# Kernel optimization log

Measured on AMD Instinct MI355X. Metric: run time of the kernel, lower is better.

The kernel has to match this reference:

```python
import jax, jax.numpy as jnp
import numpy as np

N_AGENTS = 16
NE = 128
ED = 96          # entity_shape (entity_last_action=False)
HE = 128         # hypernet_embed
MD = 32          # mixing_embed_dim
NH = 4           # attn heads
HD = HE // NH
BS, T = 32, 50


def setup_inputs() -> dict:
    key = jax.random.key(0)
    ks = jax.random.split(key, 20)
    def lin(k, i, o):
        return (jax.random.normal(k, (i, o), jnp.float32) / np.sqrt(i)).astype(jnp.float32)
    inp = {
        "agent_qs": jax.random.normal(ks[0], (BS, T, N_AGENTS), jnp.float32),
        "entities": jax.random.normal(ks[1], (BS, T, NE, ED), jnp.float32),
        "entity_mask": jax.random.uniform(ks[2], (BS, T, NE)) < 0.15,  # True = masked/inactive
    }
    for i, p in enumerate(["w1", "v"]):
        b = 3 + i * 6
        inp[p + "_fc1_w"] = lin(ks[b], ED, HE)
        inp[p + "_fc1_b"] = jnp.zeros((HE,), jnp.float32)
        inp[p + "_attn_in_w"] = lin(ks[b + 1], HE, 3 * HE)   # in_trans (no bias)
        inp[p + "_attn_out_w"] = lin(ks[b + 2], HE, HE)
        inp[p + "_attn_out_b"] = jnp.zeros((HE,), jnp.float32)
        inp[p + "_fc2_w"] = lin(ks[b + 3], HE, MD)
        inp[p + "_fc2_b"] = jnp.zeros((MD,), jnp.float32)
    return inp


def _hypernet(x, emask, fc1_w, fc1_b, in_w, out_w, out_b, fc2_w, fc2_b, mode):
    # x: [B, ne, ed], emask: [B, ne] bool (True = masked)
    B = x.shape[0]
    x1 = jax.nn.relu(x @ fc1_w + fc1_b)                         # [B, ne, HE]
    agent_mask = emask[:, :N_AGENTS]                            # [B, na]
    af = agent_mask.astype(x.dtype)
    ef = emask.astype(x.dtype)
    # attn_mask = 1 - (1-agent)(1-entity); 1 => masked pair
    pre = (1.0 - (1.0 - af)[:, :, None] * (1.0 - ef)[:, None, :]) > 0.5  # [B, na, ne]
    qkv = x1 @ in_w                                             # [B, ne, 3*HE]
    q, k, v = jnp.split(qkv, 3, axis=-1)
    q = q[:, :N_AGENTS].reshape(B, N_AGENTS, NH, HD)
    k = k.reshape(B, NE, NH, HD)
    v = v.reshape(B, NE, NH, HD)
    logits = jnp.einsum('bqhd,bkhd->bhqk', q, k) / np.float32(np.sqrt(HD))
    logits = jnp.where(pre[:, None], jnp.float32(-1e9), logits)
    w = jax.nn.softmax(logits, axis=-1)                         # [B, NH, na, ne]
    # rows where every entity is masked: torch softmax gives NaN -> filled with 0
    all_masked = jnp.all(pre, axis=-1)                          # [B, na]
    w = jnp.where(all_masked[:, None, :, None], 0.0, w)
    attn = jnp.einsum('bhqk,bkhd->bqhd', w, v).reshape(B, N_AGENTS, HE)
    out = attn @ out_w + out_b
    out = jnp.where(agent_mask[:, :, None], 0.0, out)           # post_mask fill
    x3 = out @ fc2_w + fc2_b
    x3 = jnp.where(agent_mask[:, :, None], 0.0, x3)             # [B, na, MD]
    if mode == 'alt_vector':
        return x3.mean(axis=2)                                  # [B, na]
    return x3.mean(axis=(1, 2))                                 # [B]  (scalar mode)


def reference(agent_qs, entities, entity_mask,
              w1_fc1_w, w1_fc1_b, w1_attn_in_w, w1_attn_out_w, w1_attn_out_b, w1_fc2_w, w1_fc2_b,
              v_fc1_w, v_fc1_b, v_attn_in_w, v_attn_out_w, v_attn_out_b, v_fc2_w, v_fc2_b):
    bs, max_t, ne, ed = entities.shape
    ents = entities.reshape(bs * max_t, ne, ed)
    emask = entity_mask.reshape(bs * max_t, ne)
    qs = agent_qs.reshape(-1, N_AGENTS)
    w1 = _hypernet(ents, emask, w1_fc1_w, w1_fc1_b, w1_attn_in_w, w1_attn_out_w,
                   w1_attn_out_b, w1_fc2_w, w1_fc2_b, 'alt_vector')   # [B, na]
    w1 = jnp.abs(w1)                                            # softmax_mixing_weights=False
    v = _hypernet(ents, emask, v_fc1_w, v_fc1_b, v_attn_in_w, v_attn_out_w,
                  v_attn_out_b, v_fc2_w, v_fc2_b, 'scalar')     # [B]
    q_tot = (qs * w1).sum(axis=1) + v
    return q_tot.reshape(bs, max_t, 1)
```

## Files before the change

kernel.cpp:

```cpp
#include <hip/hip_runtime.h>


#define NA 16
#define NEn 128
#define EDm 96
#define ST 136

typedef __attribute__((ext_vector_type(8))) short bf16x8;
typedef __attribute__((ext_vector_type(4))) float f32x4;

#define MFMA(a, b, c) __builtin_amdgcn_mfma_f32_16x16x32_bf16((a), (b), (c), 0, 0, 0)

#define OFF_W1 0
#define OFF_WQ 12288
#define OFF_WK 28672
#define OFF_WV 45056
#define OFF_WO 61440
#define OFF_W2 77824
#define HYPE 81920
#define WS_FLAG_OFF 327680

__device__ __forceinline__ unsigned short f2bf(float f) {
  unsigned u = __float_as_uint(f);
  u += 0x7fffu + ((u >> 16) & 1u);
  return (unsigned short)(u >> 16);
}

__device__ __forceinline__ void ctile_store(unsigned short* dst, int row0,
                                            int col, f32x4 v) {
  unsigned short m0 = f2bf(v[0]), m1 = f2bf(v[1]), m2 = f2bf(v[2]),
                 m3 = f2bf(v[3]);
  unsigned x = (unsigned)m0 | ((unsigned)m1 << 16);
  unsigned y = (unsigned)m2 | ((unsigned)m3 << 16);
  unsigned ox = (unsigned)__shfl_xor((int)x, 1);
  unsigned oy = (unsigned)__shfl_xor((int)y, 1);
  unsigned w0, w1;
  int ra;
  if ((threadIdx.x & 1) == 0) {
    ra = 0;
    w0 = (x & 0xffffu) | (ox << 16);
    w1 = (x >> 16) | (ox & 0xffff0000u);
  } else {
    ra = 2;
    w0 = (oy & 0xffffu) | (y << 16);
    w1 = (oy >> 16) | (y & 0xffff0000u);
  }
  *(unsigned*)(dst + (row0 + ra) * ST + (col & ~1)) = w0;
  *(unsigned*)(dst + (row0 + ra + 1) * ST + (col & ~1)) = w1;
}

__global__ void prep_kernel(const float* __restrict__ w_fc1w,
                            const float* __restrict__ w_inw,
                            const float* __restrict__ w_outw,
                            const float* __restrict__ w_fc2w,
                            const float* __restrict__ v_fc1w,
                            const float* __restrict__ v_inw,
                            const float* __restrict__ v_outw,
                            const float* __restrict__ v_fc2w,
                            const unsigned char* __restrict__ mask,
                            unsigned short* __restrict__ ws,
                            int* __restrict__ flag) {
  if (blockIdx.x == 160) {
    const uint4 v = *(const uint4*)(mask + threadIdx.x * 16);
    const unsigned nz = (v.x | v.y | v.z | v.w) & 0xffffff00u;
    const int any = __syncthreads_or((int)(nz != 0));
    if (threadIdx.x == 0) *flag = (any == 0) ? 1 : 0;
    return;
  }
  const int g = blockIdx.x * 256 + threadIdx.x;
  const int p = (g >= 20480) ? 1 : 0;
  const int off = (g - p * 20480) * 4;
  const float* fc1w = p ? v_fc1w : w_fc1w;
  const float* inw = p ? v_inw : w_inw;
  const float* outw = p ? v_outw : w_outw;
  const float* fc2w = p ? v_fc2w : w_fc2w;
  unsigned short* wsp = ws + p * HYPE;

  float4 v4;
  if (off < OFF_WQ) {
    v4 = *(const float4*)(fc1w + off);
#pragma unroll
    for (int r = 0; r < 4; ++r) {
      const int oe = off + r;
      const int k = oe >> 7, n = oe & 127;
      const int kt = k >> 5, kr = k & 31, j = kr & 7, khi = kr >> 3;
      const int nt = n >> 4, lo = n & 15;
      wsp[OFF_W1 + (nt * 3 + kt) * 512 + (khi * 16 + lo) * 8 + j] =
          f2bf(((const float*)&v4)[r]);
    }
  } else if (off < OFF_WK) {
    const int i = off - OFF_WQ;
    v4 = *(const float4*)(inw + (i >> 7) * 384 + (i & 127));
#pragma unroll
    for (int r = 0; r < 4; ++r) {
      const int ie = i + r;
      const int k = ie >> 7, n = ie & 127;
      const int kt = k >> 5, kr = k & 31, j = kr & 7, khi = kr >> 3;
      const int nt = n >> 4, lo = n & 15;
      wsp[OFF_WQ + (nt * 4 + kt) * 512 + (khi * 16 + lo) * 8 + j] =
          f2bf(((const float*)&v4)[r] * 0.17677669529663687f);
    }
  } else if (off < OFF_WV) {
    const int i = off - OFF_WK;
    v4 = *(const float4*)(inw + (i >> 7) * 384 + 128 + (i & 127));
#pragma unroll
    for (int r = 0; r < 4; ++r) {
      const int ie = i + r;
      const int m = ie >> 7, c = ie & 127;
      const int h = c >> 5, d = c & 31;
      const int nt = m >> 4;
      const int l = (d >> 3) * 16 + (m & 15);
      wsp[OFF_WK + (h * 8 + nt) * 512 + l * 8 + (d & 7)] =
          f2bf(((const float*)&v4)[r]);
    }
  } else if (off < OFF_WO) {
    const int i = off - OFF_WV;
    v4 = *(const float4*)(inw + (i >> 7) * 384 + 256 + (i & 127));
#pragma unroll
    for (int r = 0; r < 4; ++r) {
      const int ie = i + r;
      const int m = ie >> 7, c = ie & 127;
      const int h = c >> 5, d = c & 31;
      const int kt = m >> 5, mr = m & 31, j = mr & 7, mhi = mr >> 3;
      const int mt = d >> 4, lo = d & 15;
      wsp[OFF_WV + ((h * 2 + mt) * 4 + kt) * 512 + (mhi * 16 + lo) * 8 + j] =
          f2bf(((const float*)&v4)[r]);
    }
  } else if (off < OFF_W2) {
    const int i = off - OFF_WO;
    v4 = *(const float4*)(outw + i);
#pragma unroll
    for (int r = 0; r < 4; ++r) {
      const int ie = i + r;
      const int k = ie >> 7, n = ie & 127;
      const int kt = k >> 5, kr = k & 31, j = kr & 7, khi = kr >> 3;
      const int nt = n >> 4, lo = n & 15;
      wsp[OFF_WO + (nt * 4 + kt) * 512 + (khi * 16 + lo) * 8 + j] =
          f2bf(((const float*)&v4)[r]);
    }
  } else {
    const int i = off - OFF_W2;
    v4 = *(const float4*)(fc2w + i);
#pragma unroll
    for (int r = 0; r < 4; ++r) {
      const int ie = i + r;
      const int k = ie >> 5, n = ie & 31;
      const int kt = k >> 5, kr = k & 31, j = kr & 7, khi = kr >> 3;
      const int nt = n >> 4, lo = n & 15;
      wsp[OFF_W2 + (nt * 4 + kt) * 512 + (khi * 16 + lo) * 8 + j] =
          f2bf(((const float*)&v4)[r]);
    }
  }
}

#define SMEM_BYTES 61696

__global__ __launch_bounds__(256, 2) void qmix_mfma(
    const float* __restrict__ agent_qs, const float* __restrict__ entities,
    const unsigned char* __restrict__ emask_g,
    const unsigned short* __restrict__ wsw, const int* __restrict__ mflag,
    const float* __restrict__ w_fc1b, const float* __restrict__ w_outb,
    const float* __restrict__ w_fc2b, const float* __restrict__ v_fc1b,
    const float* __restrict__ v_outb, const float* __restrict__ v_fc2b,
    float* __restrict__ out_g) {
  const int t = threadIdx.x;
  const int wv = t >> 6;
  const int ln = t & 63;
  const int lr = ln & 15;
  const int lq = ln >> 4;
  const int b = blockIdx.x;
  const float* ents = entities + (size_t)b * (NEn * EDm);

  __shared__ __align__(16) unsigned char smem[SMEM_BYTES];
  unsigned short* sx1 = (unsigned short*)smem;
  unsigned short* sQ = sx1 + 17408;
  unsigned short* sqw = sx1 + 19584;
  unsigned short* sW = sx1 + 21760;
  unsigned short* sVT = sx1 + 23936;
  unsigned short* sattn = sx1 + 28288;
  float2* sred = (float2*)(smem + 60928);
  float* sredf = (float*)(smem + 60928);
  float* sres = (float*)(smem + 61440);
  unsigned char* sm = smem + 61568;

  const int is_i32 = *mflag;
  int mv = 1;
  if (t < NEn) {
    if (is_i32)
      mv = (((const int*)emask_g)[(size_t)b * NEn + t] != 0) ? 1 : 0;
    else
      mv = (emask_g[(size_t)b * NEn + t] != 0) ? 1 : 0;
    sm[t] = (unsigned char)mv;
  }
  const int allE = __syncthreads_and(mv);

  for (int p = 0; p < 2; ++p) {
    const unsigned short* wsb = wsw + (size_t)p * HYPE;
    const float* fc1b = p ? v_fc1b : w_fc1b;
    const float* outb = p ? v_outb : w_outb;
    const float* fc2b = p ? v_fc2b : w_fc2b;

    {
#pragma unroll
      for (int mi = 0; mi < 2; ++mi) {
        const int mt = wv * 2 + mi;
        bf16x8 af[3];
        const float* erow = ents + (mt * 16 + lr) * EDm + lq * 8;
#pragma unroll
        for (int kt = 0; kt < 3; ++kt) {
          float4 u = *(const float4*)(erow + kt * 32);
          float4 v = *(const float4*)(erow + kt * 32 + 4);
          bf16x8 a;
          a[0] = (short)f2bf(u.x); a[1] = (short)f2bf(u.y);
          a[2] = (short)f2bf(u.z); a[3] = (short)f2bf(u.w);
          a[4] = (short)f2bf(v.x); a[5] = (short)f2bf(v.y);
          a[6] = (short)f2bf(v.z); a[7] = (short)f2bf(v.w);
          af[kt] = a;
        }
        for (int nt = 0; nt < 8; ++nt) {
          f32x4 acc = {0.f, 0.f, 0.f, 0.f};
          const unsigned short* bp = wsb + OFF_W1 + (nt * 3) * 512 + ln * 8;
#pragma unroll
          for (int kt = 0; kt < 3; ++kt)
            acc = MFMA(af[kt], *(const bf16x8*)(bp + kt * 512), acc);
          const float bias = fc1b[nt * 16 + lr];
          f32x4 r;
          r[0] = fmaxf(acc[0] + bias, 0.f); r[1] = fmaxf(acc[1] + bias, 0.f);
          r[2] = fmaxf(acc[2] + bias, 0.f); r[3] = fmaxf(acc[3] + bias, 0.f);
          ctile_store(sx1, mt * 16 + lq * 4, nt * 16 + lr, r);
        }
      }
    }
    __syncthreads();

    {
      bf16x8 aq[4];
#pragma unroll
      for (int kt = 0; kt < 4; ++kt)
        aq[kt] = *(const bf16x8*)(sx1 + lr * ST + kt * 32 + lq * 8);
#pragma unroll
      for (int ni = 0; ni < 2; ++ni) {
        const int nt = wv * 2 + ni;
        f32x4 acc = {0.f, 0.f, 0.f, 0.f};
        const unsigned short* bp = wsb + OFF_WQ + (nt * 4) * 512 + ln * 8;
#pragma unroll
        for (int kt = 0; kt < 4; ++kt)
          acc = MFMA(aq[kt], *(const bf16x8*)(bp + kt * 512), acc);
        ctile_store(sQ, lq * 4, nt * 16 + lr, acc);
      }
    }
    __syncthreads();

    for (int h = 0; h < 4; ++h) {
      {
        bf16x8 aQ = *(const bf16x8*)(sQ + lr * ST + h * 32 + lq * 8);
#pragma unroll
        for (int ni = 0; ni < 2; ++ni) {
          const int nt = wv * 2 + ni;
          bf16x8 bk =
              *(const bf16x8*)(wsb + OFF_WK + (h * 8 + nt) * 512 + ln * 8);
          f32x4 acc = {0.f, 0.f, 0.f, 0.f};
          acc = MFMA(aQ, bk, acc);
          ctile_store(sqw, lq * 4, nt * 16 + lr, acc);
        }
        bf16x8 av[2][4];
#pragma unroll
        for (int mt = 0; mt < 2; ++mt)
#pragma unroll
          for (int kt = 0; kt < 4; ++kt)
            av[mt][kt] = *(const bf16x8*)(wsb + OFF_WV +
                                          (((h * 2 + mt) * 4) + kt) * 512 +
                                          ln * 8);
#pragma unroll
        for (int ni = 0; ni < 2; ++ni) {
          const int nt = wv * 2 + ni;
          bf16x8 bx[4];
#pragma unroll
          for (int kt = 0; kt < 4; ++kt)
            bx[kt] =
                *(const bf16x8*)(sx1 + (nt * 16 + lr) * ST + kt * 32 + lq * 8);
#pragma unroll
          for (int mt = 0; mt < 2; ++mt) {
            f32x4 acc = {0.f, 0.f, 0.f, 0.f};
#pragma unroll
            for (int kt = 0; kt < 4; ++kt) acc = MFMA(av[mt][kt], bx[kt], acc);
            ctile_store(sVT, mt * 16 + lq * 4, nt * 16 + lr, acc);
          }
        }
      }
      __syncthreads();

      float mx[4], ex0[4], ex1[4];
      {
        bf16x8 aw[4];
#pragma unroll
        for (int kt = 0; kt < 4; ++kt)
          aw[kt] = *(const bf16x8*)(sqw + lr * ST + kt * 32 + lq * 8);
        f32x4 a0 = {0.f, 0.f, 0.f, 0.f}, a1 = {0.f, 0.f, 0.f, 0.f};
        const int nt0 = wv * 2, nt1 = nt0 + 1;
#pragma unroll
        for (int kt = 0; kt < 4; ++kt) {
          bf16x8 b0 =
              *(const bf16x8*)(sx1 + (nt0 * 16 + lr) * ST + kt * 32 + lq * 8);
          bf16x8 b1 =
              *(const bf16x8*)(sx1 + (nt1 * 16 + lr) * ST + kt * 32 + lq * 8);
          a0 = MFMA(aw[kt], b0, a0);
          a1 = MFMA(aw[kt], b1, a1);
        }
        const int e0m = sm[nt0 * 16 + lr], e1m = sm[nt1 * 16 + lr];
        float l0[4], l1[4];
#pragma unroll
        for (int r = 0; r < 4; ++r) {
          l0[r] = e0m ? -1e9f : a0[r];
          l1[r] = e1m ? -1e9f : a1[r];
          mx[r] = fmaxf(l0[r], l1[r]);
        }
#pragma unroll
        for (int k = 1; k < 16; k <<= 1)
#pragma unroll
          for (int r = 0; r < 4; ++r)
            mx[r] = fmaxf(mx[r], __shfl_xor(mx[r], k));
        float sl[4];
#pragma unroll
        for (int r = 0; r < 4; ++r) {
          ex0[r] = __expf(l0[r] - mx[r]);
          ex1[r] = __expf(l1[r] - mx[r]);
          sl[r] = ex0[r] + ex1[r];
        }
#pragma unroll
        for (int k = 1; k < 16; k <<= 1)
#pragma unroll
          for (int r = 0; r < 4; ++r) sl[r] += __shfl_xor(sl[r], k);
        if (lr == 0) {
#pragma unroll
          for (int r = 0; r < 4; ++r)
            sred[wv * 16 + lq * 4 + r] = make_float2(mx[r], sl[r]);
        }
      }
      __syncthreads();

      {
        f32x4 w0v, w1v;
#pragma unroll
        for (int r = 0; r < 4; ++r) {
          const int row = lq * 4 + r;
          float2 p0 = sred[row], p1 = sred[16 + row], p2 = sred[32 + row],
                 p3 = sred[48 + row];
          float M = fmaxf(fmaxf(p0.x, p1.x), fmaxf(p2.x, p3.x));
          float S = __expf(p0.x - M) * p0.y + __expf(p1.x - M) * p1.y +
                    __expf(p2.x - M) * p2.y + __expf(p3.x - M) * p3.y;
          const float sc = ((int)sm[row] | allE) ? 0.f : (1.f / S);
          const float f = __expf(mx[r] - M) * sc;
          w0v[r] = ex0[r] * f;
          w1v[r] = ex1[r] * f;
        }
        ctile_store(sW, lq * 4, wv * 32 + lr, w0v);
        ctile_store(sW, lq * 4, wv * 32 + 16 + lr, w1v);
      }
      __syncthreads();

      if (wv < 2) {
        bf16x8 afr[4];
#pragma unroll
        for (int kt = 0; kt < 4; ++kt)
          afr[kt] = *(const bf16x8*)(sW + lr * ST + kt * 32 + lq * 8);
        f32x4 acc = {0.f, 0.f, 0.f, 0.f};
#pragma unroll
        for (int kt = 0; kt < 4; ++kt) {
          bf16x8 bfr =
              *(const bf16x8*)(sVT + (wv * 16 + lr) * ST + kt * 32 + lq * 8);
          acc = MFMA(afr[kt], bfr, acc);
        }
        ctile_store(sattn, lq * 4, h * 32 + wv * 16 + lr, acc);
      }
      __syncthreads();
    }

    {
      bf16x8 aa[4];
#pragma unroll
      for (int kt = 0; kt < 4; ++kt)
        aa[kt] = *(const bf16x8*)(sattn + lr * ST + kt * 32 + lq * 8);
#pragma unroll
      for (int ni = 0; ni < 2; ++ni) {
        const int nt = wv * 2 + ni;
        f32x4 acc = {0.f, 0.f, 0.f, 0.f};
        const unsigned short* bp = wsb + OFF_WO + (nt * 4) * 512 + ln * 8;
#pragma unroll
        for (int kt = 0; kt < 4; ++kt)
          acc = MFMA(aa[kt], *(const bf16x8*)(bp + kt * 512), acc);
        const float bj = outb[nt * 16 + lr];
        f32x4 r;
        r[0] = acc[0] + bj; r[1] = acc[1] + bj;
        r[2] = acc[2] + bj; r[3] = acc[3] + bj;
        ctile_store(sQ, lq * 4, nt * 16 + lr, r);
      }
    }
    __syncthreads();

    if (wv < 2) {
      bf16x8 ao[4];
#pragma unroll
      for (int kt = 0; kt < 4; ++kt)
        ao[kt] = *(const bf16x8*)(sQ + lr * ST + kt * 32 + lq * 8);
      f32x4 acc = {0.f, 0.f, 0.f, 0.f};
      const unsigned short* bp = wsb + OFF_W2 + (wv * 4) * 512 + ln * 8;
#pragma unroll
      for (int kt = 0; kt < 4; ++kt)
        acc = MFMA(ao[kt], *(const bf16x8*)(bp + kt * 512), acc);
      const float bc = fc2b[wv * 16 + lr];
      float rs[4];
#pragma unroll
      for (int r = 0; r < 4; ++r) {
        const int row = lq * 4 + r;
        rs[r] = sm[row] ? 0.f : (acc[r] + bc);
      }
#pragma unroll
      for (int k = 1; k < 16; k <<= 1)
#pragma unroll
        for (int r = 0; r < 4; ++r) rs[r] += __shfl_xor(rs[r], k);
      if (lr == 0) {
#pragma unroll
        for (int r = 0; r < 4; ++r) sredf[wv * 16 + lq * 4 + r] = rs[r];
      }
    }
    __syncthreads();
    if (t < 16) {
      const float s = sredf[t] + sredf[16 + t];
      if (p == 0)
        sres[t] = fabsf(s) * (1.f / 32.f);
      else
        sres[16 + t] = s;
    }
    __syncthreads();
  }

  if (t == 0) {
    const float* qs = agent_qs + (size_t)b * NA;
    float tot = 0.f, vs = 0.f;
#pragma unroll
    for (int q = 0; q < NA; ++q) {
      tot += qs[q] * sres[q];
      vs += sres[16 + q];
    }
    out_g[b] = tot + vs * (1.f / 512.f);
  }
}

extern "C" void kernel_launch(void* const* d_in, const int* in_sizes, int n_in,
                              void* d_out, int out_size, void* d_ws,
                              size_t ws_size, hipStream_t stream) {
  (void)n_in; (void)out_size; (void)ws_size;
  const int nb = in_sizes[0] / NA;
  unsigned short* wsw = (unsigned short*)d_ws;
  int* mflag = (int*)((char*)d_ws + WS_FLAG_OFF);

  hipLaunchKernelGGL(prep_kernel, dim3(161), dim3(256), 0, stream,
                     (const float*)d_in[3], (const float*)d_in[5],
                     (const float*)d_in[6], (const float*)d_in[8],
                     (const float*)d_in[10], (const float*)d_in[12],
                     (const float*)d_in[13], (const float*)d_in[15],
                     (const unsigned char*)d_in[2], wsw, mflag);
  hipLaunchKernelGGL(qmix_mfma, dim3(nb), dim3(256), 0, stream,
                     (const float*)d_in[0], (const float*)d_in[1],
                     (const unsigned char*)d_in[2], (const unsigned short*)wsw,
                     (const int*)mflag, (const float*)d_in[4],
                     (const float*)d_in[7], (const float*)d_in[9],
                     (const float*)d_in[11], (const float*)d_in[14],
                     (const float*)d_in[16], (float*)d_out);
}
```

Before: 302.3 us.

## Assign one attention head per wave and drop per-head block barriers

The per-head loop, where all four waves split each head's work and synchronise several times per head, is replaced by a scheme where each wave computes one full head: Q slice, key projection, logits, softmax, V projection and attention output. Intermediates live in wave-private LDS slices and are ordered with lgkmcnt waits instead of block-wide barriers, so cross-wave softmax reductions disappear. The final fc2 reduction is computed redundantly by every wave to remove two more barriers. The cost is more registers per wave (arrays of 8 and 16 accumulator tiles) and V^T written over the x1 buffer, which could reduce occupancy.

After: 268.6 us. -11.1%, faster.

```diff
diff --git a/kernel.cpp b/kernel.cpp
--- a/kernel.cpp
+++ b/kernel.cpp
@@ -10,6 +10,7 @@
 typedef __attribute__((ext_vector_type(4))) float f32x4;
 
 #define MFMA(a, b, c) __builtin_amdgcn_mfma_f32_16x16x32_bf16((a), (b), (c), 0, 0, 0)
+#define LGKM0() __asm__ volatile("s_waitcnt lgkmcnt(0)" ::: "memory")
 
 #define OFF_W1 0
 #define OFF_WQ 12288
@@ -153,7 +154,7 @@
   }
 }
 
-#define SMEM_BYTES 61696
+#define SMEM_BYTES 61184
 
 __global__ __launch_bounds__(256, 2) void qmix_mfma(
     const float* __restrict__ agent_qs, const float* __restrict__ entities,
@@ -173,15 +174,12 @@
 
   __shared__ __align__(16) unsigned char smem[SMEM_BYTES];
   unsigned short* sx1 = (unsigned short*)smem;
-  unsigned short* sQ = sx1 + 17408;
-  unsigned short* sqw = sx1 + 19584;
-  unsigned short* sW = sx1 + 21760;
-  unsigned short* sVT = sx1 + 23936;
-  unsigned short* sattn = sx1 + 28288;
-  float2* sred = (float2*)(smem + 60928);
-  float* sredf = (float*)(smem + 60928);
-  float* sres = (float*)(smem + 61440);
-  unsigned char* sm = smem + 61568;
+  unsigned short* sSlice = sx1 + 17408;
+  unsigned short* sattn = sx1 + 26112;
+  unsigned short* sout = sx1 + 28288;
+  float* sres = (float*)(smem + 60928);
+  unsigned char* sm = smem + 61056;
+  unsigned short* sS = sSlice + wv * 16 * ST;
 
   const int is_i32 = *mflag;
   int mv = 1;
@@ -246,135 +244,142 @@
 #pragma unroll
         for (int kt = 0; kt < 4; ++kt)
           acc = MFMA(aq[kt], *(const bf16x8*)(bp + kt * 512), acc);
-        ctile_store(sQ, lq * 4, nt * 16 + lr, acc);
+        ctile_store(sS, lq * 4, ni * 16 + lr, acc);
+      }
+    }
+    LGKM0();
+    const bf16x8 aQ = *(const bf16x8*)(sS + lr * ST + lq * 8);
+
+    {
+      f32x4 Cw[8];
+#pragma unroll
+      for (int nt = 0; nt < 8; ++nt) {
+        f32x4 acc = {0.f, 0.f, 0.f, 0.f};
+        Cw[nt] = MFMA(aQ, *(const bf16x8*)(wsb + OFF_WK + (wv * 8 + nt) * 512 +
+                                           ln * 8),
+                      acc);
+      }
+#pragma unroll
+      for (int nt = 0; nt < 8; ++nt)
+        ctile_store(sS, lq * 4, nt * 16 + lr, Cw[nt]);
+    }
+    LGKM0();
+    bf16x8 aw[4];
+#pragma unroll
+    for (int kt = 0; kt < 4; ++kt)
+      aw[kt] = *(const bf16x8*)(sS + lr * ST + kt * 32 + lq * 8);
+
+    f32x4 Cl[8];
+#pragma unroll
+    for (int nt = 0; nt < 8; ++nt) {
+      f32x4 acc = {0.f, 0.f, 0.f, 0.f};
+#pragma unroll
+      for (int kt = 0; kt < 4; ++kt) {
+        const bf16x8 bx =
+            *(const bf16x8*)(sx1 + (nt * 16 + lr) * ST + kt * 32 + lq * 8);
+        acc = MFMA(aw[kt], bx, acc);
+      }
+      Cl[nt] = acc;
+    }
+
+    {
+      float lv[8][4];
+#pragma unroll
+      for (int nt = 0; nt < 8; ++nt) {
+        const int eM = sm[nt * 16 + lr];
+#pragma unroll
+        for (int r = 0; r < 4; ++r) lv[nt][r] = eM ? -1e9f : Cl[nt][r];
+      }
+      float mx[4], sl[4];
+#pragma unroll
+      for (int r = 0; r < 4; ++r) {
+        float m = lv[0][r];
+#pragma unroll
+        for (int nt = 1; nt < 8; ++nt) m = fmaxf(m, lv[nt][r]);
+        mx[r] = m;
+      }
+#pragma unroll
+      for (int k = 1; k < 16; k <<= 1)
+#pragma unroll
+        for (int r = 0; r < 4; ++r) mx[r] = fmaxf(mx[r], __shfl_xor(mx[r], k));
+      float ex[8][4];
+#pragma unroll
+      for (int r = 0; r < 4; ++r) sl[r] = 0.f;
+#pragma unroll
+      for (int nt = 0; nt < 8; ++nt)
+#pragma unroll
+        for (int r = 0; r < 4; ++r) {
+          ex[nt][r] = __expf(lv[nt][r] - mx[r]);
+          sl[r] += ex[nt][r];
+        }
+#pragma unroll
+      for (int k = 1; k < 16; k <<= 1)
+#pragma unroll
+        for (int r = 0; r < 4; ++r) sl[r] += __shfl_xor(sl[r], k);
+      float sc[4];
+#pragma unroll
+      for (int r = 0; r < 4; ++r)
+        sc[r] = ((int)sm[lq * 4 + r] | allE) ? 0.f : (1.f / sl[r]);
+#pragma unroll
+      for (int nt = 0; nt < 8; ++nt) {
+        f32x4 wv4;
+#pragma unroll
+        for (int r = 0; r < 4; ++r) wv4[r] = ex[nt][r] * sc[r];
+        ctile_store(sS, lq * 4, nt * 16 + lr, wv4);
+      }
+    }
+    LGKM0();
+    bf16x8 aw2[4];
+#pragma unroll
+    for (int kt = 0; kt < 4; ++kt)
+      aw2[kt] = *(const bf16x8*)(sS + lr * ST + kt * 32 + lq * 8);
+
+    f32x4 Cv[2][8];
+#pragma unroll
+    for (int mt = 0; mt < 2; ++mt) {
+      bf16x8 av[4];
+#pragma unroll
+      for (int kt = 0; kt < 4; ++kt)
+        av[kt] = *(const bf16x8*)(wsb + OFF_WV +
+                                  (((wv * 2 + mt) * 4) + kt) * 512 + ln * 8);
+#pragma unroll
+      for (int nt = 0; nt < 8; ++nt) {
+        f32x4 acc = {0.f, 0.f, 0.f, 0.f};
+#pragma unroll
+        for (int kt = 0; kt < 4; ++kt) {
+          const bf16x8 bx =
+              *(const bf16x8*)(sx1 + (nt * 16 + lr) * ST + kt * 32 + lq * 8);
+          acc = MFMA(av[kt], bx, acc);
+        }
+        Cv[mt][nt] = acc;
       }
     }
     __syncthreads();
 
-    for (int h = 0; h < 4; ++h) {
-      {
-        bf16x8 aQ = *(const bf16x8*)(sQ + lr * ST + h * 32 + lq * 8);
-#pragma unroll
-        for (int ni = 0; ni < 2; ++ni) {
-          const int nt = wv * 2 + ni;
-          bf16x8 bk =
-              *(const bf16x8*)(wsb + OFF_WK + (h * 8 + nt) * 512 + ln * 8);
-          f32x4 acc = {0.f, 0.f, 0.f, 0.f};
-          acc = MFMA(aQ, bk, acc);
-          ctile_store(sqw, lq * 4, nt * 16 + lr, acc);
-        }
-        bf16x8 av[2][4];
-#pragma unroll
-        for (int mt = 0; mt < 2; ++mt)
-#pragma unroll
-          for (int kt = 0; kt < 4; ++kt)
-            av[mt][kt] = *(const bf16x8*)(wsb + OFF_WV +
-                                          (((h * 2 + mt) * 4) + kt) * 512 +
-                                          ln * 8);
-#pragma unroll
-        for (int ni = 0; ni < 2; ++ni) {
-          const int nt = wv * 2 + ni;
-          bf16x8 bx[4];
-#pragma unroll
-          for (int kt = 0; kt < 4; ++kt)
-            bx[kt] =
-                *(const bf16x8*)(sx1 + (nt * 16 + lr) * ST + kt * 32 + lq * 8);
-#pragma unroll
-          for (int mt = 0; mt < 2; ++mt) {
-            f32x4 acc = {0.f, 0.f, 0.f, 0.f};
-#pragma unroll
-            for (int kt = 0; kt < 4; ++kt) acc = MFMA(av[mt][kt], bx[kt], acc);
-            ctile_store(sVT, mt * 16 + lq * 4, nt * 16 + lr, acc);
-          }
-        }
-      }
-      __syncthreads();
-
-      float mx[4], ex0[4], ex1[4];
-      {
-        bf16x8 aw[4];
-#pragma unroll
-        for (int kt = 0; kt < 4; ++kt)
-          aw[kt] = *(const bf16x8*)(sqw + lr * ST + kt * 32 + lq * 8);
-        f32x4 a0 = {0.f, 0.f, 0.f, 0.f}, a1 = {0.f, 0.f, 0.f, 0.f};
-        const int nt0 = wv * 2, nt1 = nt0 + 1;
+    {
+#pragma unroll
+      for (int mt = 0; mt < 2; ++mt)
+#pragma unroll
+        for (int nt = 0; nt < 8; ++nt)
+          ctile_store(sx1, wv * 32 + mt * 16 + lq * 4, nt * 16 + lr,
+                      Cv[mt][nt]);
+    }
+    LGKM0();
+    {
+#pragma unroll
+      for (int ntd = 0; ntd < 2; ++ntd) {
+        f32x4 acc = {0.f, 0.f, 0.f, 0.f};
 #pragma unroll
         for (int kt = 0; kt < 4; ++kt) {
-          bf16x8 b0 =
-              *(const bf16x8*)(sx1 + (nt0 * 16 + lr) * ST + kt * 32 + lq * 8);
-          bf16x8 b1 =
-              *(const bf16x8*)(sx1 + (nt1 * 16 + lr) * ST + kt * 32 + lq * 8);
-          a0 = MFMA(aw[kt], b0, a0);
-          a1 = MFMA(aw[kt], b1, a1);
-        }
-        const int e0m = sm[nt0 * 16 + lr], e1m = sm[nt1 * 16 + lr];
-        float l0[4], l1[4];
-#pragma unroll
-        for (int r = 0; r < 4; ++r) {
-          l0[r] = e0m ? -1e9f : a0[r];
-          l1[r] = e1m ? -1e9f : a1[r];
-          mx[r] = fmaxf(l0[r], l1[r]);
-        }
-#pragma unroll
-        for (int k = 1; k < 16; k <<= 1)
-#pragma unroll
-          for (int r = 0; r < 4; ++r)
-            mx[r] = fmaxf(mx[r], __shfl_xor(mx[r], k));
-        float sl[4];
-#pragma unroll
-        for (int r = 0; r < 4; ++r) {
-          ex0[r] = __expf(l0[r] - mx[r]);
-          ex1[r] = __expf(l1[r] - mx[r]);
-          sl[r] = ex0[r] + ex1[r];
-        }
-#pragma unroll
-        for (int k = 1; k < 16; k <<= 1)
-#pragma unroll
-          for (int r = 0; r < 4; ++r) sl[r] += __shfl_xor(sl[r], k);
-        if (lr == 0) {
-#pragma unroll
-          for (int r = 0; r < 4; ++r)
-            sred[wv * 16 + lq * 4 + r] = make_float2(mx[r], sl[r]);
-        }
-      }
-      __syncthreads();
-
-      {
-        f32x4 w0v, w1v;
-#pragma unroll
-        for (int r = 0; r < 4; ++r) {
-          const int row = lq * 4 + r;
-          float2 p0 = sred[row], p1 = sred[16 + row], p2 = sred[32 + row],
-                 p3 = sred[48 + row];
-          float M = fmaxf(fmaxf(p0.x, p1.x), fmaxf(p2.x, p3.x));
-          float S = __expf(p0.x - M) * p0.y + __expf(p1.x - M) * p1.y +
-                    __expf(p2.x - M) * p2.y + __expf(p3.x - M) * p3.y;
-          const float sc = ((int)sm[row] | allE) ? 0.f : (1.f / S);
-          const float f = __expf(mx[r] - M) * sc;
-          w0v[r] = ex0[r] * f;
-          w1v[r] = ex1[r] * f;
-        }
-        ctile_store(sW, lq * 4, wv * 32 + lr, w0v);
-        ctile_store(sW, lq * 4, wv * 32 + 16 + lr, w1v);
-      }
-      __syncthreads();
-
-      if (wv < 2) {
-        bf16x8 afr[4];
-#pragma unroll
-        for (int kt = 0; kt < 4; ++kt)
-          afr[kt] = *(const bf16x8*)(sW + lr * ST + kt * 32 + lq * 8);
-        f32x4 acc = {0.f, 0.f, 0.f, 0.f};
-#pragma unroll
-        for (int kt = 0; kt < 4; ++kt) {
-          bf16x8 bfr =
-              *(const bf16x8*)(sVT + (wv * 16 + lr) * ST + kt * 32 + lq * 8);
-          acc = MFMA(afr[kt], bfr, acc);
-        }
-        ctile_store(sattn, lq * 4, h * 32 + wv * 16 + lr, acc);
-      }
-      __syncthreads();
-    }
+          const bf16x8 bv = *(const bf16x8*)(sx1 + (wv * 32 + ntd * 16 + lr) *
+                                                       ST +
+                                             kt * 32 + lq * 8);
+          acc = MFMA(aw2[kt], bv, acc);
+        }
+        ctile_store(sattn, lq * 4, wv * 32 + ntd * 16 + lr, acc);
+      }
+    }
+    __syncthreads();
 
     {
       bf16x8 aa[4];
@@ -393,48 +398,48 @@
         f32x4 r;
         r[0] = acc[0] + bj; r[1] = acc[1] + bj;
         r[2] = acc[2] + bj; r[3] = acc[3] + bj;
-        ctile_store(sQ, lq * 4, nt * 16 + lr, r);
+        ctile_store(sout, lq * 4, nt * 16 + lr, r);
       }
     }
     __syncthreads();
 
-    if (wv < 2) {
+    {
       bf16x8 ao[4];
 #pragma unroll
       for (int kt = 0; kt < 4; ++kt)
-        ao[kt] = *(const bf16x8*)(sQ + lr * ST + kt * 32 + lq * 8);
-      f32x4 acc = {0.f, 0.f, 0.f, 0.f};
-      const unsigned short* bp = wsb + OFF_W2 + (wv * 4) * 512 + ln * 8;
-#pragma unroll
-      for (int kt = 0; kt < 4; ++kt)
-        acc = MFMA(ao[kt], *(const bf16x8*)(bp + kt * 512), acc);
-      const float bc = fc2b[wv * 16 + lr];
+        ao[kt] = *(const bf16x8*)(sout + lr * ST + kt * 32 + lq * 8);
+      f32x4 Cx[2];
+#pragma unroll
+      for (int nt = 0; nt < 2; ++nt) {
+        f32x4 acc = {0.f, 0.f, 0.f, 0.f};
+        const unsigned short* bp = wsb + OFF_W2 + (nt * 4) * 512 + ln * 8;
+#pragma unroll
+        for (int kt = 0; kt < 4; ++kt)
+          acc = MFMA(ao[kt], *(const bf16x8*)(bp + kt * 512), acc);
+        Cx[nt] = acc;
+      }
+      const float b0 = fc2b[lr], b1 = fc2b[16 + lr];
       float rs[4];
 #pragma unroll
       for (int r = 0; r < 4; ++r) {
         const int row = lq * 4 + r;
-        rs[r] = sm[row] ? 0.f : (acc[r] + bc);
+        rs[r] = sm[row] ? 0.f : (Cx[0][r] + b0 + Cx[1][r] + b1);
       }
 #pragma unroll
       for (int k = 1; k < 16; k <<= 1)
 #pragma unroll
         for (int r = 0; r < 4; ++r) rs[r] += __shfl_xor(rs[r], k);
-      if (lr == 0) {
-#pragma unroll
-        for (int r = 0; r < 4; ++r) sredf[wv * 16 + lq * 4 + r] = rs[r];
-      }
-    }
-    __syncthreads();
-    if (t < 16) {
-      const float s = sredf[t] + sredf[16 + t];
-      if (p == 0)
-        sres[t] = fabsf(s) * (1.f / 32.f);
-      else
-        sres[16 + t] = s;
-    }
-    __syncthreads();
-  }
-
+      if (wv == 0 && lr == 0) {
+#pragma unroll
+        for (int r = 0; r < 4; ++r) {
+          const int q = lq * 4 + r;
+          sres[p * 16 + q] = p ? rs[r] : fabsf(rs[r]) * (1.f / 32.f);
+        }
+      }
+    }
+  }
+
+  __syncthreads();
   if (t == 0) {
     const float* qs = agent_qs + (size_t)b * NA;
     float tot = 0.f, vs = 0.f;
```
